# Kernel tuning notes

Hardware: AMD Instinct MI355X
Metric: run time of the kernel (lower is better)

The kernel has to match this reference:

```python
import jax, jax.numpy as jnp
import numpy as np

B, C, S, H, W = 2, 128, 64, 128, 512
MID = 32
EPS = 1e-5


def layer_norm(x, g, b):
    m = jnp.mean(x, axis=-1, keepdims=True)
    v = jnp.var(x, axis=-1, keepdims=True)
    return (x - m) / jnp.sqrt(v + EPS) * g + b


def generate_y_for_attn(s, y, u):
    # y: [B, Cy, H, W], u: [B, s, s] int indices into W (clamped)
    b, cy, h, w = y.shape
    u = jnp.clip(u, 0, w - 1)
    yr = y.reshape(b, cy * h, w)
    idx = u.reshape(b, s * s)
    g = jax.vmap(lambda m, i: m[:, i])(yr, idx)          # [B, Cy*H, s^2]
    return g.reshape(b, cy, h, s * s).transpose(0, 3, 2, 1)  # [B, s^2, H, Cy]


def setup_inputs():
    key = jax.random.key(0)
    ks = jax.random.split(key, 10)
    lim = 1.0 / np.sqrt(C)
    return {
        "sat_x": jax.random.normal(ks[0], (B, C, S, S), jnp.float32),
        "grd_x": jax.random.normal(ks[1], (B, C, H, W), jnp.float32),
        "grd_height": jax.random.normal(ks[2], (B, 1, H, W), jnp.float32),
        "u": jax.random.randint(ks[3], (B, S, S), 0, W, jnp.int32),
        "ln_q_g": jnp.ones((C,), jnp.float32),
        "ln_q_b": jnp.zeros((C,), jnp.float32),
        "wq": jax.random.uniform(ks[4], (C, MID), jnp.float32, -lim, lim),
        "bq": jax.random.uniform(ks[5], (MID,), jnp.float32, -lim, lim),
        "ln_k_g": jnp.ones((C,), jnp.float32),
        "ln_k_b": jnp.zeros((C,), jnp.float32),
        "wk": jax.random.uniform(ks[6], (C, MID), jnp.float32, -lim, lim),
        "bk": jax.random.uniform(ks[7], (MID,), jnp.float32, -lim, lim),
    }


def reference(sat_x, grd_x, grd_height, u, ln_q_g, ln_q_b, wq, bq, ln_k_g, ln_k_b, wk, bk):
    b, c, s, _ = sat_x.shape
    scale = MID ** (-0.5)
    y_attn = generate_y_for_attn(s, grd_x, u)        # [B, S^2, H, C]
    v_attn = generate_y_for_attn(s, grd_height, u)   # [B, S^2, H, 1]
    x = sat_x.reshape(b, c, s * s).transpose(0, 2, 1)  # [B, M, C]
    q = layer_norm(x, ln_q_g, ln_q_b) @ wq + bq        # [B, M, 32]
    k = layer_norm(y_attn, ln_k_g, ln_k_b) @ wk + bk   # [B, M, H, 32]
    dot = scale * jnp.einsum("bmd,bmnd->bmn", q, k)    # [B, M, H]
    att = jax.nn.softmax(dot, axis=-1)
    a = jnp.sum(att[..., None] * v_attn, axis=-2)      # [B, M, 1]
    return a.transpose(0, 2, 1).reshape(b, 1, s, s)
```

## Files before the change

kernel.cpp:

```cpp
#include <hip/hip_runtime.h>
#include <math.h>

#define B_   2
#define C_   128
#define S_   64
#define H_   128
#define W_   512
#define M_   (S_ * S_)
#define MID_ 32
#define EPS_ 1e-5f
#define CAP_ 192

#define KB3 (B_ * H_ * (W_ / 64))
#define QB3 (B_ * (M_ / 64))

__global__ __launch_bounds__(256) void proj_kernel(
    const float* __restrict__ grd_x,
    const float* __restrict__ sat_x,
    const float* __restrict__ ln_k_g, const float* __restrict__ ln_k_b,
    const float* __restrict__ wk, const float* __restrict__ bk,
    const float* __restrict__ ln_q_g, const float* __restrict__ ln_q_b,
    const float* __restrict__ wq, const float* __restrict__ bq,
    float* __restrict__ kw,
    float* __restrict__ qv)
{
    __shared__ float4 accS[4][64][4];
    __shared__ float2 sAB[4][64];
    __shared__ float  gwP[8][32], bwP[8][32];
    __shared__ float  gwS[MID_], bwS[MID_];
    __shared__ float  msS[64], rsS[64];

    const int tid  = threadIdx.x;
    const int lane = tid & 63;
    const int wv   = __builtin_amdgcn_readfirstlane(tid >> 6);
    const int blk  = blockIdx.x;
    const bool is_k = (blk < KB3);

    const float* gl   = is_k ? ln_k_g : ln_q_g;
    const float* bl   = is_k ? ln_k_b : ln_q_b;
    const float* wt   = is_k ? wk     : wq;
    const float* bias = is_k ? bk     : bq;

    int b, h = 0, pos0;
    const float* xbase;
    size_t xstr;
    if (is_k) {
        const int wchunk = blk & 7;
        h    = (blk >> 3) & (H_ - 1);
        b    = blk >> 10;
        pos0 = wchunk * 64;
        xbase = grd_x + (size_t)b * C_ * H_ * W_ + (size_t)h * W_ + pos0 + lane;
        xstr  = (size_t)H_ * W_;
    } else {
        const int qblk = blk - KB3;
        b    = qblk >> 6;
        pos0 = (qblk & 63) * 64;
        xbase = sat_x + (size_t)b * C_ * M_ + pos0 + lane;
        xstr  = (size_t)M_;
    }

    {
        const int j  = tid & 31;
        const int ch = tid >> 5;
        const float* wp = wt + (size_t)(ch * 16) * MID_ + j;
        float a = 0.f, c2 = 0.f;
#pragma unroll
        for (int i = 0; i < 16; ++i) {
            const float wvv = wp[(size_t)i * MID_];
            a  = fmaf(gl[ch * 16 + i], wvv, a);
            c2 = fmaf(bl[ch * 16 + i], wvv, c2);
        }
        gwP[ch][j] = a;
        bwP[ch][j] = c2;
    }

    const float* xp   = xbase + (size_t)(wv * 32) * xstr;
    const float* wrow = wt + (size_t)(wv * 32) * MID_;
    const float* grow = gl + wv * 32;

    float acc[MID_];
#pragma unroll
    for (int j = 0; j < MID_; ++j) acc[j] = 0.f;
    float s1 = 0.f, s2 = 0.f;

    float xv[2][8];
#pragma unroll
    for (int i = 0; i < 8; ++i) xv[0][i] = xp[(size_t)i * xstr];

    for (int g = 0; g < 4; ++g) {
        if (g < 3) {
#pragma unroll
            for (int i = 0; i < 8; ++i)
                xv[(g + 1) & 1][i] = xp[(size_t)((g + 1) * 8 + i) * xstr];
        }
#pragma unroll
        for (int i = 0; i < 8; ++i) {
            const int   cl = g * 8 + i;
            const float x  = xv[g & 1][i];
            s1 += x;
            s2  = fmaf(x, x, s2);
            const float xg = x * grow[cl];
            const float* wr = wrow + cl * MID_;
#pragma unroll
            for (int j = 0; j < MID_; ++j)
                acc[j] = fmaf(xg, wr[j], acc[j]);
        }
    }

    sAB[wv][lane] = make_float2(s1, s2);
#pragma unroll
    for (int j4 = 0; j4 < 4; ++j4)
        accS[wv][lane][(j4 + lane) & 3] =
            make_float4(acc[j4 * 4 + 0], acc[j4 * 4 + 1],
                        acc[j4 * 4 + 2], acc[j4 * 4 + 3]);
    __syncthreads();

    if (tid < 64) {
        float a = 0.f, c2 = 0.f;
#pragma unroll
        for (int w2 = 0; w2 < 4; ++w2) { a += sAB[w2][tid].x; c2 += sAB[w2][tid].y; }
        const float mean = a * (1.f / C_);
        const float var  = fmaf(-mean, mean, c2 * (1.f / C_));
        msS[tid] = mean;
        rsS[tid] = rsqrtf(var + EPS_);
    } else if (tid < 96) {
        const int j = tid - 64;
        float a = 0.f;
#pragma unroll
        for (int ch = 0; ch < 8; ++ch) a += gwP[ch][j];
        gwS[j] = a;
    } else if (tid < 128) {
        const int j = tid - 96;
        float a = 0.f;
#pragma unroll
        for (int ch = 0; ch < 8; ++ch) a += bwP[ch][j];
        bwS[j] = a + bias[j];
    }
    __syncthreads();

    const int pos = tid >> 2;
    const int jq  = tid & 3;
    float* orow;
    if (is_k) orow = kw + (((size_t)b * W_ + pos0 + pos) * H_ + h) * MID_;
    else      orow = qv + ((size_t)(b << 12) + pos0 + pos) * MID_;
    const float mean = msS[pos];
    const float rstd = rsS[pos];

    {
        float4 r = accS[0][pos][(jq + pos) & 3];
#pragma unroll
        for (int w2 = 1; w2 < 4; ++w2) {
            const float4 t = accS[w2][pos][(jq + pos) & 3];
            r.x += t.x; r.y += t.y; r.z += t.z; r.w += t.w;
        }
        const int j0 = jq * 4;
        float4 o;
        o.x = fmaf(rstd, r.x - mean * gwS[j0 + 0], bwS[j0 + 0]);
        o.y = fmaf(rstd, r.y - mean * gwS[j0 + 1], bwS[j0 + 1]);
        o.z = fmaf(rstd, r.z - mean * gwS[j0 + 2], bwS[j0 + 2]);
        o.w = fmaf(rstd, r.w - mean * gwS[j0 + 3], bwS[j0 + 3]);
        *(float4*)(orow + j0) = o;
    }
    __syncthreads();

#pragma unroll
    for (int j4 = 0; j4 < 4; ++j4)
        accS[wv][lane][(j4 + lane) & 3] =
            make_float4(acc[16 + j4 * 4 + 0], acc[16 + j4 * 4 + 1],
                        acc[16 + j4 * 4 + 2], acc[16 + j4 * 4 + 3]);
    __syncthreads();

    {
        float4 r = accS[0][pos][(jq + pos) & 3];
#pragma unroll
        for (int w2 = 1; w2 < 4; ++w2) {
            const float4 t = accS[w2][pos][(jq + pos) & 3];
            r.x += t.x; r.y += t.y; r.z += t.z; r.w += t.w;
        }
        const int j0 = 16 + jq * 4;
        float4 o;
        o.x = fmaf(rstd, r.x - mean * gwS[j0 + 0], bwS[j0 + 0]);
        o.y = fmaf(rstd, r.y - mean * gwS[j0 + 1], bwS[j0 + 1]);
        o.z = fmaf(rstd, r.z - mean * gwS[j0 + 2], bwS[j0 + 2]);
        o.w = fmaf(rstd, r.w - mean * gwS[j0 + 3], bwS[j0 + 3]);
        *(float4*)(orow + j0) = o;
    }
}

__global__ __launch_bounds__(256) void count_kernel(
    const int*   __restrict__ u,
    const float* __restrict__ qv,
    const float* __restrict__ kw,
    const float* __restrict__ gh,
    int* __restrict__ counts,
    int* __restrict__ bucket,
    float* __restrict__ out)
{
    const int bm = blockIdx.x * 256 + threadIdx.x;
    const int b  = bm >> 12;
    int w = u[bm];
    w = min(max(w, 0), W_ - 1);
    const int bw  = b * W_ + w;
    const int pos = atomicAdd(&counts[bw], 1);
    if (pos < CAP_) {
        bucket[bw * CAP_ + pos] = bm;
    } else {
        const float* qr = qv + (size_t)bm * MID_;
        const float* kr = kw + (size_t)bw * H_ * MID_;
        float mx = -1e30f, s = 0.f, sv = 0.f;
        for (int h = 0; h < H_; ++h) {
            float d = 0.f;
            for (int j = 0; j < MID_; ++j) d = fmaf(qr[j], kr[h * MID_ + j], d);
            d *= 0.17677669529663687f;
            const float nm   = fmaxf(mx, d);
            const float corr = __expf(mx - nm);
            const float e    = __expf(d - nm);
            s  = fmaf(s,  corr, e);
            sv = fmaf(sv, corr, e * gh[((size_t)b * H_ + h) * W_ + w]);
            mx = nm;
        }
        out[bm] = sv / s;
    }
}

__global__ __launch_bounds__(256) void battn_kernel(
    const float* __restrict__ qv,
    const float* __restrict__ kw,
    const float* __restrict__ gh,
    const int*   __restrict__ counts,
    const int*   __restrict__ bucket,
    float* __restrict__ out)
{
    const int blk = blockIdx.x;
    const int n   = min(counts[blk], CAP_);
    const int tid  = threadIdx.x;
    const int lane = tid & 63;
    const int wv   = __builtin_amdgcn_readfirstlane(tid >> 6);
    if (wv >= n) return;

    const int b = blk >> 9;
    const int w = blk & (W_ - 1);

    const float4* k4 = (const float4*)(kw + (size_t)blk * H_ * MID_);
    float4 ka[8], kb[8];
#pragma unroll
    for (int j = 0; j < 8; ++j) ka[j] = k4[lane * 8 + j];
#pragma unroll
    for (int j = 0; j < 8; ++j) kb[j] = k4[(lane + 64) * 8 + j];

    const float v0 = gh[((size_t)b * H_ + lane) * W_ + w];
    const float v1 = gh[((size_t)b * H_ + lane + 64) * W_ + w];

    const int* bkt = bucket + (size_t)blk * CAP_;
    const float sc = 0.17677669529663687f;

    for (int i = wv; i < n; i += 4) {
        const int bm = bkt[i];
        const float* qr = qv + (size_t)bm * MID_;
        float sq[MID_];
#pragma unroll
        for (int j = 0; j < MID_; ++j) sq[j] = qr[j];

        float d0 = 0.f, d1 = 0.f;
#pragma unroll
        for (int j = 0; j < 8; ++j) {
            d0 = fmaf(sq[j * 4 + 0], ka[j].x, d0);
            d0 = fmaf(sq[j * 4 + 1], ka[j].y, d0);
            d0 = fmaf(sq[j * 4 + 2], ka[j].z, d0);
            d0 = fmaf(sq[j * 4 + 3], ka[j].w, d0);
            d1 = fmaf(sq[j * 4 + 0], kb[j].x, d1);
            d1 = fmaf(sq[j * 4 + 1], kb[j].y, d1);
            d1 = fmaf(sq[j * 4 + 2], kb[j].z, d1);
            d1 = fmaf(sq[j * 4 + 3], kb[j].w, d1);
        }
        d0 *= sc; d1 *= sc;

        float mx = fmaxf(d0, d1);
#pragma unroll
        for (int o = 32; o > 0; o >>= 1) mx = fmaxf(mx, __shfl_xor(mx, o, 64));

        const float e0 = __expf(d0 - mx);
        const float e1 = __expf(d1 - mx);
        float s   = e0 + e1;
        float svv = fmaf(e0, v0, e1 * v1);
#pragma unroll
        for (int o = 32; o > 0; o >>= 1) {
            s   += __shfl_xor(s,   o, 64);
            svv += __shfl_xor(svv, o, 64);
        }

        if (lane == 0) out[bm] = svv / s;
    }
}

extern "C" void kernel_launch(void* const* d_in, const int* in_sizes, int n_in,
                              void* d_out, int out_size, void* d_ws, size_t ws_size,
                              hipStream_t stream) {
    const float* sat_x      = (const float*)d_in[0];
    const float* grd_x      = (const float*)d_in[1];
    const float* grd_height = (const float*)d_in[2];
    const int*   u          = (const int*)d_in[3];
    const float* ln_q_g     = (const float*)d_in[4];
    const float* ln_q_b     = (const float*)d_in[5];
    const float* wq         = (const float*)d_in[6];
    const float* bq         = (const float*)d_in[7];
    const float* ln_k_g     = (const float*)d_in[8];
    const float* ln_k_b     = (const float*)d_in[9];
    const float* wk         = (const float*)d_in[10];
    const float* bk         = (const float*)d_in[11];

    float* out = (float*)d_out;

    char* ws = (char*)d_ws;
    float* kw     = (float*)ws;
    float* q      = (float*)(ws + (size_t)16 * 1024 * 1024);
    int*   counts = (int*)  (ws + (size_t)17 * 1024 * 1024);
    int*   bucket = counts + B_ * W_;

    hipMemsetAsync(counts, 0, B_ * W_ * sizeof(int), stream);

    proj_kernel<<<KB3 + QB3, 256, 0, stream>>>(
        grd_x, sat_x, ln_k_g, ln_k_b, wk, bk, ln_q_g, ln_q_b, wq, bq, kw, q);
    count_kernel<<<(B_ * M_) / 256, 256, 0, stream>>>(
        u, q, kw, grd_height, counts, bucket, out);
    battn_kernel<<<B_ * W_, 256, 0, stream>>>(
        q, kw, grd_height, counts, bucket, out);
}
```

Baseline: 153.9 us.

## Precompute LN-folded weight sums in a prep kernel, replacing memset and per-block recompute

A new two-block prep kernel computes the gamma-weighted and beta-weighted column sums of the projection weights once and writes them to a workspace buffer. The same kernel also zeroes the counts array, which removes the separate memset call. The projection kernel no longer recomputes these sums in every block, and it loads all 32 channel values up front instead of double-buffering in groups of 8. The cost is an extra kernel launch and higher register pressure from the fully unrolled load.

Result: slower. 163.5 us (+6.3%).

```diff
diff --git a/kernel.cpp b/kernel.cpp
--- a/kernel.cpp
+++ b/kernel.cpp
@@ -14,20 +14,59 @@
 #define KB3 (B_ * H_ * (W_ / 64))
 #define QB3 (B_ * (M_ / 64))
 
-__global__ __launch_bounds__(256) void proj_kernel(
-    const float* __restrict__ grd_x,
-    const float* __restrict__ sat_x,
+__global__ __launch_bounds__(256) void prep_kernel(
     const float* __restrict__ ln_k_g, const float* __restrict__ ln_k_b,
     const float* __restrict__ wk, const float* __restrict__ bk,
     const float* __restrict__ ln_q_g, const float* __restrict__ ln_q_b,
     const float* __restrict__ wq, const float* __restrict__ bq,
+    float* __restrict__ prepbuf,
+    int* __restrict__ counts)
+{
+    const int tid = threadIdx.x;
+    const int blk = blockIdx.x;
+    const float* g    = blk ? ln_q_g : ln_k_g;
+    const float* bl   = blk ? ln_q_b : ln_k_b;
+    const float* wt   = blk ? wq     : wk;
+    const float* bias = blk ? bq     : bk;
+
+    __shared__ float pa[256], pb[256];
+
+    float a = 0.f, c2 = 0.f;
+#pragma unroll
+    for (int k = 0; k < 16; ++k) {
+        const int idx = tid + 256 * k;
+        const float wv = wt[idx];
+        const int c = idx >> 5;
+        a  = fmaf(g[c],  wv, a);
+        c2 = fmaf(bl[c], wv, c2);
+    }
+    pa[tid] = a; pb[tid] = c2;
+
+    if (blk == 0) {
+        ((int4*)counts)[tid] = make_int4(0, 0, 0, 0);
+    }
+    __syncthreads();
+
+    if (tid < 32) {
+        float s = 0.f, t = 0.f;
+#pragma unroll
+        for (int r = 0; r < 8; ++r) { s += pa[tid + 32 * r]; t += pb[tid + 32 * r]; }
+        prepbuf[blk * 64 + tid]      = s;
+        prepbuf[blk * 64 + 32 + tid] = t + bias[tid];
+    }
+}
+
+__global__ __launch_bounds__(256) void proj_kernel(
+    const float* __restrict__ grd_x,
+    const float* __restrict__ sat_x,
+    const float* __restrict__ ln_k_g, const float* __restrict__ wk,
+    const float* __restrict__ ln_q_g, const float* __restrict__ wq,
+    const float* __restrict__ prepbuf,
     float* __restrict__ kw,
     float* __restrict__ qv)
 {
     __shared__ float4 accS[4][64][4];
     __shared__ float2 sAB[4][64];
-    __shared__ float  gwP[8][32], bwP[8][32];
-    __shared__ float  gwS[MID_], bwS[MID_];
     __shared__ float  msS[64], rsS[64];
 
     const int tid  = threadIdx.x;
@@ -36,10 +75,9 @@
     const int blk  = blockIdx.x;
     const bool is_k = (blk < KB3);
 
-    const float* gl   = is_k ? ln_k_g : ln_q_g;
-    const float* bl   = is_k ? ln_k_b : ln_q_b;
-    const float* wt   = is_k ? wk     : wq;
-    const float* bias = is_k ? bk     : bq;
+    const float* gl = is_k ? ln_k_g : ln_q_g;
+    const float* wt = is_k ? wk     : wq;
+    const int setoff = is_k ? 0 : 64;
 
     int b, h = 0, pos0;
     const float* xbase;
@@ -59,52 +97,29 @@
         xstr  = (size_t)M_;
     }
 
-    {
-        const int j  = tid & 31;
-        const int ch = tid >> 5;
-        const float* wp = wt + (size_t)(ch * 16) * MID_ + j;
-        float a = 0.f, c2 = 0.f;
-#pragma unroll
-        for (int i = 0; i < 16; ++i) {
-            const float wvv = wp[(size_t)i * MID_];
-            a  = fmaf(gl[ch * 16 + i], wvv, a);
-            c2 = fmaf(bl[ch * 16 + i], wvv, c2);
-        }
-        gwP[ch][j] = a;
-        bwP[ch][j] = c2;
-    }
-
     const float* xp   = xbase + (size_t)(wv * 32) * xstr;
     const float* wrow = wt + (size_t)(wv * 32) * MID_;
     const float* grow = gl + wv * 32;
 
+    float xv[32];
+#pragma unroll
+    for (int c = 0; c < 32; ++c) xv[c] = xp[(size_t)c * xstr];
+
     float acc[MID_];
 #pragma unroll
     for (int j = 0; j < MID_; ++j) acc[j] = 0.f;
     float s1 = 0.f, s2 = 0.f;
 
-    float xv[2][8];
-#pragma unroll
-    for (int i = 0; i < 8; ++i) xv[0][i] = xp[(size_t)i * xstr];
-
-    for (int g = 0; g < 4; ++g) {
-        if (g < 3) {
-#pragma unroll
-            for (int i = 0; i < 8; ++i)
-                xv[(g + 1) & 1][i] = xp[(size_t)((g + 1) * 8 + i) * xstr];
-        }
-#pragma unroll
-        for (int i = 0; i < 8; ++i) {
-            const int   cl = g * 8 + i;
-            const float x  = xv[g & 1][i];
-            s1 += x;
-            s2  = fmaf(x, x, s2);
-            const float xg = x * grow[cl];
-            const float* wr = wrow + cl * MID_;
-#pragma unroll
-            for (int j = 0; j < MID_; ++j)
-                acc[j] = fmaf(xg, wr[j], acc[j]);
-        }
+#pragma unroll
+    for (int c = 0; c < 32; ++c) {
+        const float x = xv[c];
+        s1 += x;
+        s2  = fmaf(x, x, s2);
+        const float xg = x * grow[c];
+        const float* wr = wrow + c * MID_;
+#pragma unroll
+        for (int j = 0; j < MID_; ++j)
+            acc[j] = fmaf(xg, wr[j], acc[j]);
     }
 
     sAB[wv][lane] = make_float2(s1, s2);
@@ -123,18 +138,6 @@
         const float var  = fmaf(-mean, mean, c2 * (1.f / C_));
         msS[tid] = mean;
         rsS[tid] = rsqrtf(var + EPS_);
-    } else if (tid < 96) {
-        const int j = tid - 64;
-        float a = 0.f;
-#pragma unroll
-        for (int ch = 0; ch < 8; ++ch) a += gwP[ch][j];
-        gwS[j] = a;
-    } else if (tid < 128) {
-        const int j = tid - 96;
-        float a = 0.f;
-#pragma unroll
-        for (int ch = 0; ch < 8; ++ch) a += bwP[ch][j];
-        bwS[j] = a + bias[j];
     }
     __syncthreads();
 
@@ -154,11 +157,13 @@
             r.x += t.x; r.y += t.y; r.z += t.z; r.w += t.w;
         }
         const int j0 = jq * 4;
+        const float4 gw4 = *(const float4*)(prepbuf + setoff + j0);
+        const float4 bw4 = *(const float4*)(prepbuf + setoff + 32 + j0);
         float4 o;
-        o.x = fmaf(rstd, r.x - mean * gwS[j0 + 0], bwS[j0 + 0]);
-        o.y = fmaf(rstd, r.y - mean * gwS[j0 + 1], bwS[j0 + 1]);
-        o.z = fmaf(rstd, r.z - mean * gwS[j0 + 2], bwS[j0 + 2]);
-        o.w = fmaf(rstd, r.w - mean * gwS[j0 + 3], bwS[j0 + 3]);
+        o.x = fmaf(rstd, fmaf(-mean, gw4.x, r.x), bw4.x);
+        o.y = fmaf(rstd, fmaf(-mean, gw4.y, r.y), bw4.y);
+        o.z = fmaf(rstd, fmaf(-mean, gw4.z, r.z), bw4.z);
+        o.w = fmaf(rstd, fmaf(-mean, gw4.w, r.w), bw4.w);
         *(float4*)(orow + j0) = o;
     }
     __syncthreads();
@@ -178,11 +183,13 @@
             r.x += t.x; r.y += t.y; r.z += t.z; r.w += t.w;
         }
         const int j0 = 16 + jq * 4;
+        const float4 gw4 = *(const float4*)(prepbuf + setoff + j0);
+        const float4 bw4 = *(const float4*)(prepbuf + setoff + 32 + j0);
         float4 o;
-        o.x = fmaf(rstd, r.x - mean * gwS[j0 + 0], bwS[j0 + 0]);
-        o.y = fmaf(rstd, r.y - mean * gwS[j0 + 1], bwS[j0 + 1]);
-        o.z = fmaf(rstd, r.z - mean * gwS[j0 + 2], bwS[j0 + 2]);
-        o.w = fmaf(rstd, r.w - mean * gwS[j0 + 3], bwS[j0 + 3]);
+        o.x = fmaf(rstd, fmaf(-mean, gw4.x, r.x), bw4.x);
+        o.y = fmaf(rstd, fmaf(-mean, gw4.y, r.y), bw4.y);
+        o.z = fmaf(rstd, fmaf(-mean, gw4.z, r.z), bw4.z);
+        o.w = fmaf(rstd, fmaf(-mean, gw4.w, r.w), bw4.w);
         *(float4*)(orow + j0) = o;
     }
 }
@@ -312,15 +319,16 @@
     float* out = (float*)d_out;
 
     char* ws = (char*)d_ws;
-    float* kw     = (float*)ws;
-    float* q      = (float*)(ws + (size_t)16 * 1024 * 1024);
-    int*   counts = (int*)  (ws + (size_t)17 * 1024 * 1024);
-    int*   bucket = counts + B_ * W_;
-
-    hipMemsetAsync(counts, 0, B_ * W_ * sizeof(int), stream);
-
+    float* kw      = (float*)ws;
+    float* q       = (float*)(ws + (size_t)16 * 1024 * 1024);
+    int*   counts  = (int*)  (ws + (size_t)17 * 1024 * 1024);
+    int*   bucket  = counts + B_ * W_;
+    float* prepbuf = (float*)(ws + (size_t)18 * 1024 * 1024);
+
+    prep_kernel<<<2, 256, 0, stream>>>(
+        ln_k_g, ln_k_b, wk, bk, ln_q_g, ln_q_b, wq, bq, prepbuf, counts);
     proj_kernel<<<KB3 + QB3, 256, 0, stream>>>(
-        grd_x, sat_x, ln_k_g, ln_k_b, wk, bk, ln_q_g, ln_q_b, wq, bq, kw, q);
+        grd_x, sat_x, ln_k_g, wk, ln_q_g, wq, prepbuf, kw, q);
     count_kernel<<<(B_ * M_) / 256, 256, 0, stream>>>(
         u, q, kw, grd_height, counts, bucket, out);
     battn_kernel<<<B_ * W_, 256, 0, stream>>>(
```
